# Performance work log

Hardware: AMD Instinct MI355X
Metric: run time of the kernel (lower is better)

## Reference

```python
import jax, jax.numpy as jnp
import numpy as np

# Rank1Canvas: luma conversion then per-sample rank-1 (top singular triplet) reconstruction.
# The torch original adds 1e-6 Gaussian jitter purely for SVD numerical robustness;
# it is omitted here (its effect on the output is ~1e-6 and random inputs are non-degenerate).

def setup_inputs() -> dict:
    key = jax.random.key(0)
    x = jax.random.normal(key, (32, 3, 512, 512), dtype=jnp.float32)
    return {"x": x}

def reference(x) -> jnp.ndarray:
    # x: [B, 3, H, W] -> luma [B, H, W]
    y = 0.299 * x[:, 0] + 0.587 * x[:, 1] + 0.114 * x[:, 2]
    # Batched SVD (jnp.linalg.svd vectorizes over leading dims)
    U, S, Vh = jnp.linalg.svd(y, full_matrices=False)  # U:[B,H,K] S:[B,K] Vh:[B,K,W]
    # Rank-1 reconstruction: s0 * u0 v0^T, per sample
    rank1 = S[:, 0, None, None] * jnp.einsum('bh,bw->bhw', U[:, :, 0], Vh[:, 0, :])
    return rank1[:, None]  # [B, 1, H, W]
```

## Files before the change

### kernel.cpp

```cpp
#include <hip/hip_runtime.h>
#include <hip/hip_fp16.h>

#define NB 32
#define N 512
#define MAT (N*N)

typedef _Float16 half8 __attribute__((ext_vector_type(8)));
typedef float f32x4 __attribute__((ext_vector_type(4)));

#define MSCALE 2048.0f
#define RMSCALE (1.0f/2048.0f)

__device__ inline ushort2 split2(float x) {
    __half h = __float2half(x);
    __half m = __float2half((x - __half2float(h)) * MSCALE);
    return make_ushort2(__half_as_ushort(h), __half_as_ushort(m));
}

__device__ inline void gload(const ushort* g, ushort* l) {
    __builtin_amdgcn_global_load_lds((const __attribute__((address_space(1))) void*)g,
                                     (__attribute__((address_space(3))) void*)l, 16, 0, 0);
}

__device__ inline float h2f(ushort u) {
    return __half2float(__builtin_bit_cast(__half, u));
}

__global__ __launch_bounds__(256) void k_luma(const float* __restrict__ x, float* __restrict__ yT,
                                              ushort* __restrict__ Ph, ushort* __restrict__ Pm) {
    int b = blockIdx.y;
    int tile = blockIdx.x;
    int TR = (tile >> 3) * 64;
    int TC = (tile & 7) * 64;
    __shared__ float ld[64][65];
    int t = threadIdx.x;
    int r0 = t >> 4;
    int c4 = (t & 15) * 4;
    const float* xb = x + (size_t)b * 3 * MAT;
    #pragma unroll
    for (int q = 0; q < 4; ++q) {
        int row = r0 + q * 16;
        size_t off = (size_t)(TR + row) * N + TC + c4;
        float4 rr = *(const float4*)&xb[off];
        float4 gg = *(const float4*)&xb[off + MAT];
        float4 bb = *(const float4*)&xb[off + 2 * MAT];
        ld[row][c4 + 0] = 0.299f * rr.x + 0.587f * gg.x + 0.114f * bb.x;
        ld[row][c4 + 1] = 0.299f * rr.y + 0.587f * gg.y + 0.114f * bb.y;
        ld[row][c4 + 2] = 0.299f * rr.z + 0.587f * gg.z + 0.114f * bb.z;
        ld[row][c4 + 3] = 0.299f * rr.w + 0.587f * gg.w + 0.114f * bb.w;
    }
    __syncthreads();
    float* yTb = yT + (size_t)b * MAT;
    ushort* PhB = Ph + (size_t)b * MAT;
    ushort* PmB = Pm + (size_t)b * MAT;
    #pragma unroll
    for (int q = 0; q < 4; ++q) {
        int i = r0 + q * 16;
        float v0 = ld[c4 + 0][i];
        float v1 = ld[c4 + 1][i];
        float v2 = ld[c4 + 2][i];
        float v3 = ld[c4 + 3][i];
        size_t off = (size_t)(TC + i) * N + TR + c4;
        *(float4*)&yTb[off] = make_float4(v0, v1, v2, v3);
        ushort2 s0 = split2(v0), s1 = split2(v1), s2 = split2(v2), s3 = split2(v3);
        *(ushort4*)&PhB[off] = make_ushort4(s0.x, s1.x, s2.x, s3.x);
        *(ushort4*)&PmB[off] = make_ushort4(s0.y, s1.y, s2.y, s3.y);
    }
}

template<int NPIN>
__global__ __launch_bounds__(256, 2) void k_gemm(const ushort* __restrict__ Ph, const ushort* __restrict__ Pm,
                                                 ushort* __restrict__ Qh, ushort* __restrict__ Qm,
                                                 const float* __restrict__ fsrc, float* __restrict__ fdst) {
    int bid = blockIdx.x;
    int xcd = bid & 7, q0 = bid >> 3;
    int b = xcd + 8 * (q0 >> 4);
    int tile = q0 & 15;
    const ushort* PhB = Ph + (size_t)b * MAT;
    const ushort* PmB = (NPIN == 2) ? Pm + (size_t)b * MAT : nullptr;

    __shared__ __align__(16) ushort sI[2][NPIN][128 * 32];
    __shared__ __align__(16) ushort sJ[2][NPIN][128 * 32];

    int t = threadIdx.x;
    int iBase = (tile >> 2) * 128, jBase = (tile & 3) * 128;
    bool diag = (iBase == jBase);

    int lane = t & 63, wv = t >> 6;
    int wi = wv >> 1, wj = wv & 1;
    int cc = lane & 15, cq = lane >> 4;
    int q8 = cq * 8;
    int lrow = lane >> 2;
    int lseg = lane & 3;

    float alpha = fsrc ? (1.0f / fsrc[b]) : 1.0f;

    auto stage = [&](int buf, int k0) {
        if (NPIN == 2) {
            if (diag) {
                #pragma unroll
                for (int j = 0; j < 4; ++j) {
                    int q = wv * 4 + j;
                    int pl = q >> 3, rg = q & 7;
                    const ushort* src = (pl ? PmB : PhB) + (size_t)(iBase + rg * 16 + lrow) * N + k0 + lseg * 8;
                    gload(src, &sI[buf][pl][rg * 512]);
                }
            } else {
                #pragma unroll
                for (int j = 0; j < 8; ++j) {
                    int q = wv * 8 + j;
                    int panel = q >> 4, pl = (q >> 3) & 1, rg = q & 7;
                    int rb = panel ? jBase : iBase;
                    const ushort* src = (pl ? PmB : PhB) + (size_t)(rb + rg * 16 + lrow) * N + k0 + lseg * 8;
                    gload(src, panel ? &sJ[buf][pl][rg * 512] : &sI[buf][pl][rg * 512]);
                }
            }
        } else {
            if (diag) {
                #pragma unroll
                for (int j = 0; j < 2; ++j) {
                    int rg = wv * 2 + j;
                    const ushort* src = PhB + (size_t)(iBase + rg * 16 + lrow) * N + k0 + lseg * 8;
                    gload(src, &sI[buf][0][rg * 512]);
                }
            } else {
                #pragma unroll
                for (int j = 0; j < 4; ++j) {
                    int q = wv * 4 + j;
                    int panel = q >> 3, rg = q & 7;
                    int rb = panel ? jBase : iBase;
                    const ushort* src = PhB + (size_t)(rb + rg * 16 + lrow) * N + k0 + lseg * 8;
                    gload(src, panel ? &sJ[buf][0][rg * 512] : &sI[buf][0][rg * 512]);
                }
            }
        }
    };

    f32x4 acc0[4][4], acc1[4][4];
    #pragma unroll
    for (int i = 0; i < 4; ++i)
        #pragma unroll
        for (int j = 0; j < 4; ++j) { acc0[i][j] = (f32x4)0.f; acc1[i][j] = (f32x4)0.f; }

    stage(0, 0);
    __syncthreads();

    for (int k0 = 0; k0 < N; k0 += 32) {
        int cur = (k0 >> 5) & 1;
        if (k0 + 32 < N) stage(cur ^ 1, k0 + 32);

        const ushort(*Ib)[128 * 32] = sI[cur];
        const ushort(*Jb)[128 * 32] = diag ? sI[cur] : sJ[cur];

        half8 bh[4], bm[4];
        #pragma unroll
        for (int ct = 0; ct < 4; ++ct) {
            int row = wj * 64 + ct * 16 + cc;
            bh[ct] = *(const half8*)&Jb[0][row * 32 + q8];
            if (NPIN == 2) bm[ct] = *(const half8*)&Jb[1][row * 32 + q8];
        }
        #pragma unroll
        for (int rt = 0; rt < 4; ++rt) {
            int row = wi * 64 + rt * 16 + cc;
            half8 ah = *(const half8*)&Ib[0][row * 32 + q8];
            half8 am;
            if (NPIN == 2) am = *(const half8*)&Ib[1][row * 32 + q8];
            #pragma unroll
            for (int ct = 0; ct < 4; ++ct) {
                acc0[rt][ct] = __builtin_amdgcn_mfma_f32_16x16x32_f16(ah, bh[ct], acc0[rt][ct], 0, 0, 0);
                if (NPIN == 2) {
                    acc1[rt][ct] = __builtin_amdgcn_mfma_f32_16x16x32_f16(ah, bm[ct], acc1[rt][ct], 0, 0, 0);
                    acc1[rt][ct] = __builtin_amdgcn_mfma_f32_16x16x32_f16(am, bh[ct], acc1[rt][ct], 0, 0, 0);
                }
            }
        }
        __syncthreads();
    }

    ushort* QhB = Qh + (size_t)b * MAT;
    ushort* QmB = Qm ? Qm + (size_t)b * MAT : nullptr;
    float ss = 0.f;
    #pragma unroll
    for (int rt = 0; rt < 4; ++rt) {
        int i0 = iBase + wi * 64 + rt * 16 + cq * 4;
        #pragma unroll
        for (int ct = 0; ct < 4; ++ct) {
            int j0 = jBase + wj * 64 + ct * 16 + cc;
            #pragma unroll
            for (int r = 0; r < 4; ++r) {
                float o = acc0[rt][ct][r];
                if (NPIN == 2) o += acc1[rt][ct][r] * RMSCALE;
                o *= alpha;
                ss += o * o;
                size_t idx = (size_t)(i0 + r) * N + j0;
                if (QmB) {
                    ushort2 hm = split2(o);
                    QhB[idx] = hm.x;
                    QmB[idx] = hm.y;
                } else {
                    QhB[idx] = __half_as_ushort(__float2half(o));
                }
            }
        }
    }

    if (fdst) {
        for (int o = 32; o; o >>= 1) ss += __shfl_down(ss, o, 64);
        __shared__ float red[4];
        if (lane == 0) red[wv] = ss;
        __syncthreads();
        if (t == 0) atomicAdd(&fdst[b], red[0] + red[1] + red[2] + red[3]);
    }
}

template<int MODE>
__global__ __launch_bounds__(512) void k_piter(const ushort* __restrict__ Ch, const float* __restrict__ vin,
                                               float* __restrict__ dst, float* __restrict__ ssout) {
    int b = blockIdx.y, g = blockIdx.x;
    const ushort* C = Ch + (size_t)b * MAT;
    __shared__ float sv[N];
    __shared__ float part[32][65];
    int t = threadIdx.x;
    if (MODE == 0) {
        unsigned h = (unsigned)t * 1103515245u + 12345u;
        sv[t] = (float)((h >> 16) & 0x7fff) / 16384.f - 1.f;
    } else {
        sv[t] = vin[(size_t)b * N + t];
    }
    __syncthreads();

    int lane = t & 63, e = t >> 6;
    int j4 = (lane & 15) * 4;
    int cq = lane >> 4;
    int jb = g * 64;
    float a0 = 0.f, a1 = 0.f, a2 = 0.f, a3 = 0.f;
    #pragma unroll
    for (int c = 0; c < 64; c += 4) {
        int row = e * 64 + c + cq;
        ushort4 q = *(const ushort4*)&C[(size_t)row * N + jb + j4];
        float s = sv[row];
        a0 = fmaf(h2f(q.x), s, a0);
        a1 = fmaf(h2f(q.y), s, a1);
        a2 = fmaf(h2f(q.z), s, a2);
        a3 = fmaf(h2f(q.w), s, a3);
    }
    int pr = e * 4 + cq;
    part[pr][j4 + 0] = a0;
    part[pr][j4 + 1] = a1;
    part[pr][j4 + 2] = a2;
    part[pr][j4 + 3] = a3;
    __syncthreads();
    if (t < 64) {
        float o = 0.f;
        #pragma unroll
        for (int q = 0; q < 32; ++q) o += part[q][t];
        dst[(size_t)b * N + jb + t] = o;
        if (MODE == 2) {
            float val = o * o;
            #pragma unroll
            for (int s = 32; s; s >>= 1) val += __shfl_xor(val, s, 64);
            if (t == 0) atomicAdd(&ssout[b], val);
        }
    }
}

__global__ __launch_bounds__(512) void k_wfin(const float* __restrict__ YT, const float* __restrict__ vin,
                                              const float* __restrict__ ss, float* __restrict__ vout,
                                              float* __restrict__ wout) {
    int b = blockIdx.y, g = blockIdx.x;
    const float* Yt = YT + (size_t)b * MAT;
    float rs = rsqrtf(ss[b]);
    __shared__ float sv[N];
    __shared__ float part[32][65];
    int t = threadIdx.x;
    sv[t] = vin[(size_t)b * N + t];
    __syncthreads();

    int lane = t & 63, e = t >> 6;
    int j4 = (lane & 15) * 4;
    int cq = lane >> 4;
    int jb = g * 64;
    float a0 = 0.f, a1 = 0.f, a2 = 0.f, a3 = 0.f;
    #pragma unroll
    for (int c = 0; c < 64; c += 4) {
        int row = e * 64 + c + cq;
        float4 q = *(const float4*)&Yt[(size_t)row * N + jb + j4];
        float s = sv[row];
        a0 = fmaf(q.x, s, a0);
        a1 = fmaf(q.y, s, a1);
        a2 = fmaf(q.z, s, a2);
        a3 = fmaf(q.w, s, a3);
    }
    int pr = e * 4 + cq;
    part[pr][j4 + 0] = a0;
    part[pr][j4 + 1] = a1;
    part[pr][j4 + 2] = a2;
    part[pr][j4 + 3] = a3;
    __syncthreads();
    if (t < 64) {
        float w = 0.f;
        #pragma unroll
        for (int q = 0; q < 32; ++q) w += part[q][t];
        wout[(size_t)b * N + jb + t] = w * rs;
        vout[(size_t)b * N + jb + t] = sv[jb + t] * rs;
    }
}

__global__ __launch_bounds__(256) void k_outer(const float* __restrict__ v, const float* __restrict__ w,
                                               float* __restrict__ out) {
    int tid = blockIdx.x * 256 + threadIdx.x;
    int b = tid >> 16;
    int rem = tid & 65535;
    int i = rem >> 7;
    int j4 = rem & 127;
    float wi = w[(size_t)b * N + i];
    float4 vv = ((const float4*)(v + (size_t)b * N))[j4];
    float4 o = {wi * vv.x, wi * vv.y, wi * vv.z, wi * vv.w};
    ((float4*)out)[tid] = o;
}

extern "C" void kernel_launch(void* const* d_in, const int* in_sizes, int n_in,
                              void* d_out, int out_size, void* d_ws, size_t ws_size,
                              hipStream_t stream) {
    const float* x = (const float*)d_in[0];
    float* out = (float*)d_out;
    char* base = (char*)d_ws;

    const size_t PL = (size_t)NB * MAT * sizeof(ushort);
    ushort* AH = (ushort*)(base);
    ushort* AM = (ushort*)(base + PL);
    ushort* BH = (ushort*)(base + 2 * PL);
    ushort* BM = (ushort*)(base + 3 * PL);
    float*  fs = (float*)(base + 4 * PL);
    float*  vv = fs + 512;
    float*  ww = vv + (size_t)NB * N;
    float*  v2 = ww + (size_t)NB * N;
    float*  yT = out;
    float*  ssf = fs + 256;

    hipMemsetAsync(fs, 0, 512 * sizeof(float), stream);
    k_luma<<<dim3(64, NB), 256, 0, stream>>>(x, yT, AH, AM);

    dim3 gg(512, 1, 1);
    k_gemm<2><<<gg, 256, 0, stream>>>(AH, AM, BH, BM,      nullptr,   fs + 0*32);
    k_gemm<2><<<gg, 256, 0, stream>>>(BH, BM, AH, AM,      fs + 0*32, fs + 1*32);
    k_gemm<2><<<gg, 256, 0, stream>>>(AH, AM, BH, nullptr, fs + 1*32, fs + 2*32);
    k_gemm<1><<<gg, 256, 0, stream>>>(BH, nullptr, AH, nullptr, fs + 2*32, fs + 3*32);
    k_gemm<1><<<gg, 256, 0, stream>>>(AH, nullptr, BH, nullptr, fs + 3*32, fs + 4*32);
    k_gemm<1><<<gg, 256, 0, stream>>>(BH, nullptr, AH, nullptr, fs + 4*32, fs + 5*32);
    k_gemm<1><<<gg, 256, 0, stream>>>(AH, nullptr, BH, nullptr, fs + 5*32, fs + 6*32);
    k_gemm<1><<<gg, 256, 0, stream>>>(BH, nullptr, AH, nullptr, fs + 6*32, fs + 7*32);
    k_gemm<1><<<gg, 256, 0, stream>>>(AH, nullptr, BH, nullptr, fs + 7*32, nullptr);

    dim3 gp(8, NB);
    k_piter<0><<<gp, 512, 0, stream>>>(BH, nullptr, vv, nullptr);
    k_piter<1><<<gp, 512, 0, stream>>>(BH, vv, v2, nullptr);
    k_piter<1><<<gp, 512, 0, stream>>>(BH, v2, vv, nullptr);
    k_piter<1><<<gp, 512, 0, stream>>>(BH, vv, v2, nullptr);
    k_piter<1><<<gp, 512, 0, stream>>>(BH, v2, vv, nullptr);
    k_piter<1><<<gp, 512, 0, stream>>>(BH, vv, v2, nullptr);
    k_piter<1><<<gp, 512, 0, stream>>>(BH, v2, vv, nullptr);
    k_piter<2><<<gp, 512, 0, stream>>>(BH, vv, v2, ssf);

    k_wfin<<<gp, 512, 0, stream>>>(yT, v2, ssf, vv, ww);
    k_outer<<<8192, 256, 0, stream>>>(vv, ww, out);
}
```

Measured before the change: 406.8 us.

## Triple-buffer single-plane GEMM with explicit vmcnt waits and raw barriers

For the single-precision-plane GEMM variant, the shared-memory staging grows from two to three buffers. Loads run two k-steps ahead, and completion is tracked with explicit s_waitcnt vmcnt counts plus s_barrier, replacing a full __syncthreads each iteration. The aim is to hide global-to-LDS latency behind the MFMA work and to cut how long the pipeline stalls at each barrier. In exchange it uses more LDS per block, which may reduce occupancy, and its correctness relies on the hand-set vmcnt counts matching the number of loads issued per stage.

```diff
diff --git a/kernel.cpp b/kernel.cpp
--- a/kernel.cpp
+++ b/kernel.cpp
@@ -24,6 +24,12 @@
 
 __device__ inline float h2f(ushort u) {
     return __half2float(__builtin_bit_cast(__half, u));
+}
+
+__device__ inline void wvm(int n) {
+    if (n == 0)      asm volatile("s_waitcnt vmcnt(0)" ::: "memory");
+    else if (n == 2) asm volatile("s_waitcnt vmcnt(2)" ::: "memory");
+    else             asm volatile("s_waitcnt vmcnt(4)" ::: "memory");
 }
 
 __global__ __launch_bounds__(256) void k_luma(const float* __restrict__ x, float* __restrict__ yT,
@@ -72,6 +78,7 @@
 __global__ __launch_bounds__(256, 2) void k_gemm(const ushort* __restrict__ Ph, const ushort* __restrict__ Pm,
                                                  ushort* __restrict__ Qh, ushort* __restrict__ Qm,
                                                  const float* __restrict__ fsrc, float* __restrict__ fdst) {
+    constexpr int DEPTH = (NPIN == 1) ? 3 : 2;
     int bid = blockIdx.x;
     int xcd = bid & 7, q0 = bid >> 3;
     int b = xcd + 8 * (q0 >> 4);
@@ -79,8 +86,8 @@
     const ushort* PhB = Ph + (size_t)b * MAT;
     const ushort* PmB = (NPIN == 2) ? Pm + (size_t)b * MAT : nullptr;
 
-    __shared__ __align__(16) ushort sI[2][NPIN][128 * 32];
-    __shared__ __align__(16) ushort sJ[2][NPIN][128 * 32];
+    __shared__ __align__(16) ushort sI[DEPTH][NPIN][128 * 32];
+    __shared__ __align__(16) ushort sJ[DEPTH][NPIN][128 * 32];
 
     int t = threadIdx.x;
     int iBase = (tile >> 2) * 128, jBase = (tile & 3) * 128;
@@ -142,16 +149,9 @@
         #pragma unroll
         for (int j = 0; j < 4; ++j) { acc0[i][j] = (f32x4)0.f; acc1[i][j] = (f32x4)0.f; }
 
-    stage(0, 0);
-    __syncthreads();
-
-    for (int k0 = 0; k0 < N; k0 += 32) {
-        int cur = (k0 >> 5) & 1;
-        if (k0 + 32 < N) stage(cur ^ 1, k0 + 32);
-
-        const ushort(*Ib)[128 * 32] = sI[cur];
-        const ushort(*Jb)[128 * 32] = diag ? sI[cur] : sJ[cur];
-
+    auto mac = [&](int buf) {
+        const ushort(*Ib)[128 * 32] = sI[buf];
+        const ushort(*Jb)[128 * 32] = diag ? sI[buf] : sJ[buf];
         half8 bh[4], bm[4];
         #pragma unroll
         for (int ct = 0; ct < 4; ++ct) {
@@ -174,7 +174,30 @@
                 }
             }
         }
+    };
+
+    if constexpr (DEPTH == 3) {
+        const int L = diag ? 2 : 4;
+        stage(0, 0);
+        stage(1, 32);
+        wvm(L);
+        __builtin_amdgcn_s_barrier();
+        for (int kt = 0; kt < 16; ++kt) {
+            if (kt + 2 < 16) stage((kt + 2) % 3, (kt + 2) * 32);
+            mac(kt % 3);
+            if (kt + 2 < 16) wvm(L);
+            else if (kt + 1 < 16) wvm(0);
+            if (kt + 1 < 16) __builtin_amdgcn_s_barrier();
+        }
+    } else {
+        stage(0, 0);
         __syncthreads();
+        for (int k0 = 0; k0 < N; k0 += 32) {
+            int cur = (k0 >> 5) & 1;
+            if (k0 + 32 < N) stage(cur ^ 1, k0 + 32);
+            mac(cur);
+            __syncthreads();
+        }
     }
 
     ushort* QhB = Qh + (size_t)b * MAT;
```

Result: faster. 395.1 us (-2.9%).
